# Optimization experiments

Hardware: AMD Instinct MI355X
Metric: run time of the kernel (lower is better)

## Reference

```python
import jax, jax.numpy as jnp
import numpy as np

D_MODEL = 1024
N_HEADS = 16
DFF = 4096
B, S = 2, 2048
EPS = 1e-6


def _dense_params(key, d_in, d_out):
    kw, kb = jax.random.split(key)
    w = jax.random.normal(kw, (d_in, d_out), jnp.float32) * 0.02
    b = jax.random.normal(kb, (d_out,), jnp.float32) * 0.02
    return w, b


def setup_inputs() -> dict:
    key = jax.random.key(0)
    ks = jax.random.split(key, 20)
    inp = {
        "x": jax.random.normal(ks[0], (B, S, D_MODEL), jnp.float32),
        "enc_output": jax.random.normal(ks[1], (B, S, D_MODEL), jnp.float32),
        # causal look-ahead mask: 1 where attention is NOT allowed
        "look_ahead_mask": jnp.triu(jnp.ones((S, S), jnp.float32), k=1)[None, None],
        "padding_mask": (jax.random.uniform(ks[2], (B, 1, 1, S)) < 0.1).astype(jnp.float32),
    }
    names = ["mha1_wq", "mha1_wk", "mha1_wv", "mha1_wo",
             "mha2_wq", "mha2_wk", "mha2_wv", "mha2_wo"]
    for i, n in enumerate(names):
        w, b = _dense_params(ks[3 + i], D_MODEL, D_MODEL)
        inp[n] = w
        inp[n.replace("w", "b")] = b
    inp["ffn_w1"], inp["ffn_b1"] = _dense_params(ks[11], D_MODEL, DFF)
    inp["ffn_w2"], inp["ffn_b2"] = _dense_params(ks[12], DFF, D_MODEL)
    for i, n in enumerate(["ln1", "ln2", "ln3"]):
        inp[n + "_g"] = jnp.ones((D_MODEL,), jnp.float32)
        inp[n + "_b"] = jnp.zeros((D_MODEL,), jnp.float32)
    return inp


def _layernorm(x, g, b):
    mu = jnp.mean(x, axis=-1, keepdims=True)
    var = jnp.mean(jnp.square(x - mu), axis=-1, keepdims=True)
    return (x - mu) * jax.lax.rsqrt(var + EPS) * g + b


def _mha(v, k, q, mask, wq, bq, wk, bk, wv, bv, wo, bo):
    Bq, Sq, D = q.shape
    depth = D // N_HEADS

    def split(t):  # [B,S,D] -> [B,H,S,depth]
        return t.reshape(t.shape[0], -1, N_HEADS, depth).transpose(0, 2, 1, 3)

    qh = split(q @ wq + bq)
    kh = split(k @ wk + bk)
    vh = split(v @ wv + bv)
    logits = jnp.einsum("bhqd,bhkd->bhqk", qh, kh) / jnp.sqrt(jnp.float32(depth))
    if mask is not None:
        logits = logits + mask * (-1e9)
    attn = jax.nn.softmax(logits, axis=-1)
    out = jnp.einsum("bhqk,bhkd->bhqd", attn, vh)
    out = out.transpose(0, 2, 1, 3).reshape(Bq, Sq, D)
    return out @ wo + bo


def reference(x, enc_output, look_ahead_mask, padding_mask,
              mha1_wq, mha1_bq, mha1_wk, mha1_bk, mha1_wv, mha1_bv, mha1_wo, mha1_bo,
              mha2_wq, mha2_bq, mha2_wk, mha2_bk, mha2_wv, mha2_bv, mha2_wo, mha2_bo,
              ffn_w1, ffn_b1, ffn_w2, ffn_b2,
              ln1_g, ln1_b, ln2_g, ln2_b, ln3_g, ln3_b):
    # self-attention (training=False -> dropout is identity)
    attn1 = _mha(x, x, x, look_ahead_mask,
                 mha1_wq, mha1_bq, mha1_wk, mha1_bk, mha1_wv, mha1_bv, mha1_wo, mha1_bo)
    out1 = _layernorm(x + attn1, ln1_g, ln1_b)
    # cross-attention: q from decoder, k/v from encoder output
    attn2 = _mha(enc_output, enc_output, out1, padding_mask,
                 mha2_wq, mha2_bq, mha2_wk, mha2_bk, mha2_wv, mha2_bv, mha2_wo, mha2_bo)
    out2 = _layernorm(out1 + attn2, ln2_g, ln2_b)
    ffn = jax.nn.relu(out2 @ ffn_w1 + ffn_b1) @ ffn_w2 + ffn_b2
    return _layernorm(out2 + ffn, ln3_g, ln3_b)
```

## Files before the change

kernel.cpp:

```cpp
#include <hip/hip_runtime.h>
#include <hip/hip_bf16.h>
#include <stdint.h>

#define DM   1024
#define NH   16
#define SS   2048
#define BB   2
#define MT   4096

typedef __attribute__((ext_vector_type(8))) short short8;
typedef __attribute__((ext_vector_type(4))) float f32x4;

typedef __attribute__((address_space(1))) const unsigned int as1_uint;
typedef __attribute__((address_space(3))) unsigned int as3_uint;

__device__ __forceinline__ void async16(const void* g, void* l) {
  __builtin_amdgcn_global_load_lds((as1_uint*)g, (as3_uint*)l, 16, 0, 0);
}

#define WAITV(n) asm volatile("s_waitcnt vmcnt(" #n ")" ::: "memory")
#define BARRIER_SB() do { __builtin_amdgcn_s_barrier(); __builtin_amdgcn_sched_barrier(0); } while (0)
#define EXP2(x) __builtin_amdgcn_exp2f(x)

__device__ __forceinline__ unsigned short f2bf(float f) {
  union { float f; unsigned u; } c; c.f = f;
  unsigned r = c.u + 0x7fffu + ((c.u >> 16) & 1u);
  return (unsigned short)(r >> 16);
}

__device__ __forceinline__ unsigned cvt_pk_bf16(float lo, float hi) {
  unsigned r;
  asm("v_cvt_pk_bf16_f32 %0, %1, %2" : "=v"(r) : "v"(lo), "v"(hi));
  return r;
}

__device__ __forceinline__ float swz16(float x) {
  return __uint_as_float((unsigned)__builtin_amdgcn_ds_swizzle((int)__float_as_uint(x), 0x401F));
}

__device__ __forceinline__ void xcd_swz(int& bx, int& by, int& bz) {
  int GX = gridDim.x, GY = gridDim.y;
  int nwg = GX * GY * gridDim.z;
  int old = blockIdx.x + GX * (blockIdx.y + GY * blockIdx.z);
  int f2 = (old & 7) * (nwg >> 3) + (old >> 3);
  bz = f2 / (GX * GY);
  int rem = f2 % (GX * GY);
  bx = rem / GY;
  by = rem % GY;
}

__global__ __launch_bounds__(256) void k_conv2(
    const float* __restrict__ a, const float* __restrict__ b,
    unsigned short* __restrict__ oa, unsigned short* __restrict__ ob) {
  int bxr = blockIdx.x;
  const float* in = (bxr < 4096) ? a : b;
  unsigned short* out = (bxr < 4096) ? oa : ob;
  int i = ((bxr & 4095) * 256 + threadIdx.x) * 4;
  float4 v = *(const float4*)(in + i);
  uint2 u;
  u.x = (unsigned)f2bf(v.x) | ((unsigned)f2bf(v.y) << 16);
  u.y = (unsigned)f2bf(v.z) | ((unsigned)f2bf(v.w) << 16);
  *(uint2*)(out + i) = u;
}

__global__ __launch_bounds__(256) void k_transpose_bf16(
    const float* __restrict__ in, unsigned short* __restrict__ out, int R, int C) {
  __shared__ float t[64][65];
  int c0 = blockIdx.x * 64, r0 = blockIdx.y * 64;
  int tx = threadIdx.x & 63, ty = threadIdx.x >> 6;
#pragma unroll
  for (int i = 0; i < 16; i++)
    t[ty + i * 4][tx] = in[(size_t)(r0 + ty + i * 4) * C + c0 + tx];
  __syncthreads();
#pragma unroll
  for (int i = 0; i < 16; i++)
    out[(size_t)(c0 + ty + i * 4) * R + r0 + tx] = f2bf(t[tx][ty + i * 4]);
}

struct PtrArr { const float* p[8]; };
__global__ __launch_bounds__(256) void k_transpose8(
    PtrArr ps, unsigned short* __restrict__ out0) {
  __shared__ float t[64][65];
  const float* in = ps.p[blockIdx.z];
  unsigned short* out = out0 + (size_t)blockIdx.z * 1048576;
  int c0 = blockIdx.x * 64, r0 = blockIdx.y * 64;
  int tx = threadIdx.x & 63, ty = threadIdx.x >> 6;
#pragma unroll
  for (int i = 0; i < 16; i++)
    t[ty + i * 4][tx] = in[(size_t)(r0 + ty + i * 4) * 1024 + c0 + tx];
  __syncthreads();
#pragma unroll
  for (int i = 0; i < 16; i++)
    out[(size_t)(c0 + ty + i * 4) * 1024 + r0 + tx] = f2bf(t[tx][ty + i * 4]);
}

__device__ __forceinline__ void stage_half(
    unsigned short* lds, int dst_off, const unsigned short* __restrict__ src,
    int sbase, int c0, int K, int kk, int tid) {
#pragma unroll
  for (int c = 0; c < 2; c++) {
    int e = ((c0 + c) * 512 + tid) * 8;
    int r_ = e >> 6, s_ = e & 63;
    async16(src + (size_t)(sbase + r_) * K + kk + (s_ ^ ((r_ & 4) << 2)),
            &lds[dst_off + e]);
  }
}

__device__ __forceinline__ void read_afrags(
    const unsigned short* lds, int aoff, int wm, int rh, int l15, int l4,
    short8 af[4][2]) {
#pragma unroll
  for (int i = 0; i < 4; i++) {
    int arow = wm * 128 + rh * 64 + i * 16 + l15;
#pragma unroll
    for (int ks = 0; ks < 2; ks++)
      af[i][ks] = *(const short8*)&lds[aoff + arow * 64 +
          ((ks * 32 + l4 * 8) ^ ((arow & 4) << 2))];
  }
}

__device__ __forceinline__ void read_bfrags(
    const unsigned short* lds, int boff, int wn, int ch, int l15, int l4,
    short8 bf[2][2]) {
#pragma unroll
  for (int j = 0; j < 2; j++) {
    int brw = wn * 64 + ch * 32 + j * 16 + l15;
#pragma unroll
    for (int ks = 0; ks < 2; ks++)
      bf[j][ks] = *(const short8*)&lds[boff + brw * 64 +
          ((ks * 32 + l4 * 8) ^ ((brw & 4) << 2))];
  }
}

#define MFMA_CL(RH, CH)                                                        \
  __builtin_amdgcn_s_barrier();                                                \
  asm volatile("s_waitcnt lgkmcnt(0)" ::: "memory");                           \
  __builtin_amdgcn_sched_barrier(0);                                           \
  __builtin_amdgcn_s_setprio(1);                                               \
  _Pragma("unroll")                                                            \
  for (int ks = 0; ks < 2; ks++)                                               \
    _Pragma("unroll")                                                          \
    for (int i = 0; i < 4; i++)                                                \
      _Pragma("unroll")                                                        \
      for (int j = 0; j < 2; j++)                                              \
        acc[(RH) * 4 + i][(CH) * 2 + j] =                                      \
            __builtin_amdgcn_mfma_f32_16x16x32_bf16(                           \
                af[i][ks], bf[j][ks], acc[(RH) * 4 + i][(CH) * 2 + j], 0, 0, 0); \
  __builtin_amdgcn_s_setprio(0);

template<int OUT_MODE, bool RELU>
__global__ __launch_bounds__(512, 2) void k_gemm256(
    const unsigned short* __restrict__ A,
    const unsigned short* __restrict__ Bt,
    const float* __restrict__ bias,
    void* __restrict__ p0, void* __restrict__ p1,
    void* __restrict__ p2, void* __restrict__ p3,
    int M, int N, int K, int KS) {
  extern __shared__ unsigned short lds[];
  int tid = threadIdx.x;
  int wid = tid >> 6, lane = tid & 63;
  int wm = wid >> 2, wn = wid & 3;
  int l15 = lane & 15, l4 = lane >> 4;
  int brow = blockIdx.y * 256, bcol = blockIdx.x * 256;
  int bz = blockIdx.z;
  int kbeg = bz * KS;
  int nk = KS / 64;

  f32x4 acc[8][4];
#pragma unroll
  for (int i = 0; i < 8; i++)
#pragma unroll
    for (int j = 0; j < 4; j++) acc[i][j] = (f32x4){0.f, 0.f, 0.f, 0.f};

  short8 af[4][2], bf[2][2];

  stage_half(lds, 32768, Bt, bcol, 0, K, kbeg, tid);
  stage_half(lds, 32768, Bt, bcol, 2, K, kbeg, tid);
  stage_half(lds, 0,     A,  brow, 0, K, kbeg, tid);
  stage_half(lds, 0,     A,  brow, 2, K, kbeg, tid);
  WAITV(0);
  __builtin_amdgcn_s_barrier();

  for (int t = 0; t < nk; t++) {
    int buf = t & 1, nb = buf ^ 1;
    int aoff = buf * 16384, boff = 32768 + buf * 16384;
    int naoff = nb * 16384, nboff = 32768 + nb * 16384;
    int kk2 = kbeg + (t + 1) * 64;
    bool more = (t + 1 < nk);

    read_afrags(lds, aoff, wm, 0, l15, l4, af);
    read_bfrags(lds, boff, wn, 0, l15, l4, bf);
    if (more) {
      stage_half(lds, nboff, Bt, bcol, 0, K, kk2, tid);
      stage_half(lds, nboff, Bt, bcol, 2, K, kk2, tid);
    }
    MFMA_CL(0, 0);
    __builtin_amdgcn_s_barrier();

    read_bfrags(lds, boff, wn, 1, l15, l4, bf);
    if (more) stage_half(lds, naoff, A, brow, 0, K, kk2, tid);
    MFMA_CL(0, 1);
    __builtin_amdgcn_s_barrier();

    read_afrags(lds, aoff, wm, 1, l15, l4, af);
    read_bfrags(lds, boff, wn, 0, l15, l4, bf);
    if (more) stage_half(lds, naoff, A, brow, 2, K, kk2, tid);
    MFMA_CL(1, 0);
    __builtin_amdgcn_s_barrier();

    read_bfrags(lds, boff, wn, 1, l15, l4, bf);
    MFMA_CL(1, 1);
    if (more) {
      WAITV(0);
      __builtin_amdgcn_s_barrier();
    }
  }

  if (OUT_MODE == 1) {
    unsigned short* op = (unsigned short*)p0;
#pragma unroll
    for (int ai = 0; ai < 8; ai++)
#pragma unroll
      for (int bj = 0; bj < 4; bj++) {
        int row = brow + wm * 128 + ai * 16 + l4 * 4;
        int col = bcol + wn * 64 + bj * 16 + l15;
        float bs = bias[col];
#pragma unroll
        for (int r = 0; r < 4; r++) {
          float v = acc[ai][bj][r] + bs;
          if (RELU) v = fmaxf(v, 0.f);
          op[(size_t)(row + r) * N + col] = f2bf(v);
        }
      }
  } else {
    float* op = (float*)((bz == 0) ? p0 : (bz == 1) ? p1 : (bz == 2) ? p2 : p3);
#pragma unroll
    for (int ai = 0; ai < 8; ai++)
#pragma unroll
      for (int bj = 0; bj < 4; bj++) {
        int row = brow + wm * 128 + ai * 16 + l4 * 4;
        int col = bcol + wn * 64 + bj * 16 + l15;
#pragma unroll
        for (int r = 0; r < 4; r++)
          op[(size_t)(row + r) * N + col] = acc[ai][bj][r];
      }
  }
}

template<int BM, int OUT_MODE, bool RELU, bool RESID, bool SPLITK>
__global__ __launch_bounds__(256) void k_gemm(
    const unsigned short* __restrict__ A,
    const unsigned short* __restrict__ Bt,
    const float* __restrict__ bias,
    const float* __restrict__ resid,
    void* __restrict__ outp, void* __restrict__ outp2,
    int M, int N, int K, int KS) {
  __shared__ unsigned short Alds[3][BM * 32];
  __shared__ unsigned short Blds[3][128 * 32];
  int tid = threadIdx.x;
  int w = tid >> 6, lane = tid & 63;
  int l15 = lane & 15, l4 = lane >> 4;
  int bxs, bys, bzs;
  xcd_swz(bxs, bys, bzs);
  int brow = bys * BM, bcol = bxs * 128;

  constexpr int MR = 4;
  constexpr int NR = (BM == 128) ? 4 : 2;
  int wr = (BM == 128) ? (w >> 1) : 0;
  int wc = (BM == 128) ? (w & 1) : w;
  int rbase = wr * 64;
  int cbase = wc * (NR * 16);

  f32x4 acc[MR][NR];
#pragma unroll
  for (int i = 0; i < MR; i++)
#pragma unroll
    for (int j = 0; j < NR; j++) acc[i][j] = (f32x4){0.f, 0.f, 0.f, 0.f};

#define STAGEG(bufi, kk) do {                                                  \
    _Pragma("unroll")                                                          \
    for (int c = 0; c < BM / 64; c++) {                                        \
      int elem = (c * 256 + tid) * 8;                                          \
      int row = elem >> 5, col = elem & 31;                                    \
      async16(A + (size_t)(brow + row) * K + (kk) + col, &Alds[bufi][elem]);   \
    }                                                                          \
    _Pragma("unroll")                                                          \
    for (int c = 0; c < 2; c++) {                                              \
      int elem = (c * 256 + tid) * 8;                                          \
      int row = elem >> 5, col = elem & 31;                                    \
      async16(Bt + (size_t)(bcol + row) * K + (kk) + col, &Blds[bufi][elem]);  \
    } } while (0)

  int kbeg = SPLITK ? bzs * KS : 0;
  int nk = KS / 32;
  STAGEG(0, kbeg);
  if (nk > 1) {
    STAGEG(1, kbeg + 32);
    if (BM == 128) WAITV(4); else WAITV(3);
  } else {
    WAITV(0);
  }
  BARRIER_SB();

  for (int t = 0; t < nk; t++) {
    int buf = t % 3;
    if (t + 2 < nk) STAGEG((t + 2) % 3, kbeg + (t + 2) * 32);
    short8 af[MR], bfr[NR];
#pragma unroll
    for (int i = 0; i < MR; i++)
      af[i] = *(const short8*)&Alds[buf][(rbase + i * 16 + l15) * 32 + l4 * 8];
#pragma unroll
    for (int j = 0; j < NR; j++)
      bfr[j] = *(const short8*)&Blds[buf][(cbase + j * 16 + l15) * 32 + l4 * 8];
#pragma unroll
    for (int i = 0; i < MR; i++)
#pragma unroll
      for (int j = 0; j < NR; j++)
        acc[i][j] = __builtin_amdgcn_mfma_f32_16x16x32_bf16(af[i], bfr[j], acc[i][j], 0, 0, 0);
    if (t + 2 < nk) {
      if (BM == 128) WAITV(4); else WAITV(3);
    } else if (t + 1 < nk) {
      WAITV(0);
    }
    if (t + 1 < nk) BARRIER_SB();
  }
#undef STAGEG

  void* op = (SPLITK && bzs) ? outp2 : outp;
#pragma unroll
  for (int i = 0; i < MR; i++)
#pragma unroll
    for (int j = 0; j < NR; j++) {
      int row = brow + rbase + i * 16 + l4 * 4;
      int col = bcol + cbase + j * 16 + l15;
      float bs = (SPLITK || !bias) ? 0.f : bias[col];
#pragma unroll
      for (int r = 0; r < 4; r++) {
        float v = acc[i][j][r] + bs;
        if (RESID) v += resid[(size_t)(row + r) * N + col];
        if (RELU) v = fmaxf(v, 0.f);
        if (OUT_MODE == 0) ((float*)op)[(size_t)(row + r) * N + col] = v;
        else               ((unsigned short*)op)[(size_t)(row + r) * N + col] = f2bf(v);
      }
    }
}

__global__ __launch_bounds__(256) void k_gemm_qkv(
    const unsigned short* __restrict__ a0, const unsigned short* __restrict__ a1,
    const unsigned short* __restrict__ a2,
    const unsigned short* __restrict__ Bt,
    const float* __restrict__ b0, const float* __restrict__ b1, const float* __restrict__ b2,
    unsigned short* __restrict__ o0, unsigned short* __restrict__ o1, unsigned short* __restrict__ o2,
    int vmat, int M, int K) {
  __shared__ unsigned short Alds[3][128 * 32];
  __shared__ unsigned short Blds[3][128 * 32];
  int tid = threadIdx.x;
  int w = tid >> 6, lane = tid & 63;
  int wr = w >> 1, wc = w & 1;
  int l15 = lane & 15, l4 = lane >> 4;
  int bxs, bys, z;
  xcd_swz(bxs, bys, z);
  const unsigned short* A  = (z == 0) ? a0 : (z == 1) ? a1 : a2;
  const unsigned short* Bz = Bt + (size_t)z * 1048576;
  int brow = bys * 128, bcol = bxs * 128;

  f32x4 acc[4][4];
#pragma unroll
  for (int i = 0; i < 4; i++)
#pragma unroll
    for (int j = 0; j < 4; j++) acc[i][j] = (f32x4){0.f, 0.f, 0.f, 0.f};

#define STAGEQ(bufi, kk) do {                                                  \
    _Pragma("unroll")                                                          \
    for (int c = 0; c < 2; c++) {                                              \
      int elem = (c * 256 + tid) * 8;                                          \
      int row = elem >> 5, col = elem & 31;                                    \
      async16(A + (size_t)(brow + row) * K + (kk) + col, &Alds[bufi][elem]);   \
      async16(Bz + (size_t)(bcol + row) * K + (kk) + col, &Blds[bufi][elem]);  \
    } } while (0)

  int nk = K / 32;
  STAGEQ(0, 0);
  STAGEQ(1, 32);
  WAITV(4);
  BARRIER_SB();

  for (int t = 0; t < nk; t++) {
    int buf = t % 3;
    if (t + 2 < nk) STAGEQ((t + 2) % 3, (t + 2) * 32);
    short8 af[4], bfr[4];
#pragma unroll
    for (int i = 0; i < 4; i++) {
      af[i]  = *(const short8*)&Alds[buf][(wr * 64 + i * 16 + l15) * 32 + l4 * 8];
      bfr[i] = *(const short8*)&Blds[buf][(wc * 64 + i * 16 + l15) * 32 + l4 * 8];
    }
#pragma unroll
    for (int i = 0; i < 4; i++)
#pragma unroll
      for (int j = 0; j < 4; j++)
        acc[i][j] = __builtin_amdgcn_mfma_f32_16x16x32_bf16(af[i], bfr[j], acc[i][j], 0, 0, 0);
    if (t + 2 < nk) WAITV(4);
    else if (t + 1 < nk) WAITV(0);
    if (t + 1 < nk) BARRIER_SB();
  }
#undef STAGEQ

  const float* bias = (z == 0) ? b0 : (z == 1) ? b1 : b2;
  unsigned short* op = (z == 0) ? o0 : (z == 1) ? o1 : o2;
  bool tr = (z == vmat);
#pragma unroll
  for (int i = 0; i < 4; i++)
#pragma unroll
    for (int j = 0; j < 4; j++) {
      int row = brow + wr * 64 + i * 16 + l4 * 4;
      int colL = bcol + wc * 64 + j * 16 + l15;
      float bs = bias[colL];
#pragma unroll
      for (int r = 0; r < 4; r++) {
        float v = acc[i][j][r] + bs;
        if (tr) op[(size_t)colL * M + row + r] = f2bf(v);
        else    op[(size_t)(row + r) * 1024 + colL] = f2bf(v);
      }
    }
}

template<bool CAUSAL, int NF>
__global__ __launch_bounds__(256) void k_attn(
    const unsigned short* __restrict__ Q,
    const unsigned short* __restrict__ Kb,
    const unsigned short* __restrict__ Vt,
    const float* __restrict__ pm,
    unsigned short* __restrict__ out) {
  __shared__ unsigned short Klds[3][64 * 64];
  __shared__ unsigned short Vlds[3][64 * 64];
  __shared__ unsigned short Pw[4][NF][16 * 72];
  int tid = threadIdx.x, w = tid >> 6, lane = tid & 63;
  int l15 = lane & 15, l4 = lane >> 4;
  int h = blockIdx.y, b = blockIdx.z;
  const float SC = 0.125f * 1.44269504089f;
  const int NPASS = CAUSAL ? 2 : 1;

#define STAGE(bufi, kt_) do {                                                  \
    _Pragma("unroll")                                                          \
    for (int c = 0; c < 2; c++) {                                              \
      int e0 = w * 1024 + c * 512;                                             \
      int elem = e0 + lane * 8;                                                \
      int row_ = elem >> 6;                                                    \
      int col_ = (elem & 63) ^ ((row_ & 7) << 3);                              \
      async16(Kb + (size_t)(b * SS + (kt_) * 64 + row_) * DM + h * 64 + col_,  \
              &Klds[bufi][elem]);                                              \
      async16(Vt + (size_t)(h * 64 + row_) * MT + b * SS + (kt_) * 64 + col_,  \
              &Vlds[bufi][elem]);                                              \
    } } while (0)

  for (int pass = 0; pass < NPASS; pass++) {
    int qt = CAUSAL ? (pass == 0 ? (31 - (int)blockIdx.x) : (int)blockIdx.x)
                    : (int)blockIdx.x;
    int qbase = qt * (NF * 64) + w * (NF * 16);

    short8 qf[NF][2];
#pragma unroll
    for (int f = 0; f < NF; f++) {
      size_t qrow = (size_t)b * SS + qbase + f * 16 + l15;
#pragma unroll
      for (int ks = 0; ks < 2; ks++)
        qf[f][ks] = *(const short8*)(Q + qrow * DM + h * 64 + ks * 32 + l4 * 8);
    }

    float mrow[NF], lrow[NF];
    f32x4 accO[NF][4];
#pragma unroll
    for (int f = 0; f < NF; f++) {
      mrow[f] = -1e30f; lrow[f] = 0.f;
#pragma unroll
      for (int d = 0; d < 4; d++) accO[f][d] = (f32x4){0.f, 0.f, 0.f, 0.f};
    }

    int ktend = CAUSAL ? qt : (SS / 64 - 1);
    if (pass) BARRIER_SB();
    STAGE(0, 0);
    if (ktend >= 1) { STAGE(1, 1); WAITV(4); } else { WAITV(0); }
    BARRIER_SB();

    for (int kt = 0; kt <= ktend; kt++) {
      int buf = kt % 3;
      if (kt + 2 <= ktend) STAGE((kt + 2) % 3, kt + 2);

      bool active = !CAUSAL || (kt * 64 <= qbase + NF * 16 - 1);
      if (active) {
        f32x4 sa[NF][4];
#pragma unroll
        for (int f = 0; f < NF; f++)
#pragma unroll
          for (int nt = 0; nt < 4; nt++) sa[f][nt] = (f32x4){0.f, 0.f, 0.f, 0.f};
        __builtin_amdgcn_s_setprio(1);
#pragma unroll
        for (int ks = 0; ks < 2; ks++)
#pragma unroll
          for (int nt = 0; nt < 4; nt++) {
            int kr = nt * 16 + l15;
            short8 kf = *(const short8*)&Klds[buf][kr * 64 + ((ks * 32 + l4 * 8) ^ ((kr & 7) << 3))];
#pragma unroll
            for (int f = 0; f < NF; f++)
              sa[f][nt] = __builtin_amdgcn_mfma_f32_16x16x32_bf16(kf, qf[f][ks], sa[f][nt], 0, 0, 0);
          }
        __builtin_amdgcn_s_setprio(0);

        float pmb[16];
        if (!CAUSAL) {
#pragma unroll
          for (int nt = 0; nt < 4; nt++) {
            float4 pmv = *(const float4*)(pm + b * SS + kt * 64 + nt * 16 + l4 * 4);
#pragma unroll
            for (int r = 0; r < 4; r++) pmb[nt * 4 + r] = ((const float*)&pmv)[r] * -1e30f;
          }
        }
        bool diag = CAUSAL && (kt * 64 + 63 > qbase);

        float sv[NF][16], tm[NF];
#pragma unroll
        for (int f = 0; f < NF; f++) {
          if (CAUSAL && !diag) {
#pragma unroll
            for (int i = 0; i < 16; i++) sv[f][i] = sa[f][i >> 2][i & 3] * SC;
          } else if (CAUSAL) {
#pragma unroll
            for (int nt = 0; nt < 4; nt++)
#pragma unroll
              for (int r = 0; r < 4; r++) {
                float s = sa[f][nt][r] * SC;
                int kg = kt * 64 + nt * 16 + l4 * 4 + r;
                int qg = qbase + f * 16 + l15;
                if (kg > qg) s = -1e30f;
                sv[f][nt * 4 + r] = s;
              }
          } else {
#pragma unroll
            for (int i = 0; i < 16; i++)
              sv[f][i] = fmaf(sa[f][i >> 2][i & 3], SC, pmb[i]);
          }
          float t8[8];
#pragma unroll
          for (int i = 0; i < 8; i++) t8[i] = fmaxf(sv[f][i], sv[f][i + 8]);
#pragma unroll
          for (int i = 0; i < 4; i++) t8[i] = fmaxf(t8[i], t8[i + 4]);
          t8[0] = fmaxf(t8[0], t8[1]);
          t8[2] = fmaxf(t8[2], t8[3]);
          tm[f] = fmaxf(t8[0], t8[2]);
        }

        float sA[NF];
#pragma unroll
        for (int f = 0; f < NF; f++) sA[f] = swz16(tm[f]);
#pragma unroll
        for (int f = 0; f < NF; f++) tm[f] = fmaxf(tm[f], sA[f]);
        float xA[NF];
#pragma unroll
        for (int f = 0; f < NF; f++) xA[f] = __shfl_xor(tm[f], 32);
#pragma unroll
        for (int f = 0; f < NF; f++) tm[f] = fmaxf(tm[f], xA[f]);

#pragma unroll
        for (int f = 0; f < NF; f++) {
          if (!__all(tm[f] - mrow[f] <= 8.f)) {
            float mnew = fmaxf(mrow[f], tm[f]);
            float corr = EXP2(mrow[f] - mnew);
            mrow[f] = mnew;
            lrow[f] *= corr;
#pragma unroll
            for (int r = 0; r < 4; r++) {
              float cq = __shfl(corr, l4 * 4 + r);
#pragma unroll
              for (int dt = 0; dt < 4; dt++) accO[f][dt][r] *= cq;
            }
          }

          float p[16];
#pragma unroll
          for (int i = 0; i < 16; i++) p[i] = EXP2(sv[f][i] - mrow[f]);
          float a8[8];
#pragma unroll
          for (int i = 0; i < 8; i++) a8[i] = p[i] + p[i + 8];
#pragma unroll
          for (int i = 0; i < 4; i++) a8[i] = a8[i] + a8[i + 4];
          lrow[f] += (a8[0] + a8[1]) + (a8[2] + a8[3]);

#pragma unroll
          for (int nt = 0; nt < 4; nt++) {
            uint2 u;
            u.x = cvt_pk_bf16(p[nt * 4 + 0], p[nt * 4 + 1]);
            u.y = cvt_pk_bf16(p[nt * 4 + 2], p[nt * 4 + 3]);
            *(uint2*)&Pw[w][f][l15 * 72 + nt * 16 + l4 * 4] = u;
          }
        }

        __builtin_amdgcn_s_setprio(1);
#pragma unroll
        for (int ks = 0; ks < 2; ks++) {
          short8 pf[NF];
#pragma unroll
          for (int f = 0; f < NF; f++)
            pf[f] = *(const short8*)&Pw[w][f][l15 * 72 + ks * 32 + l4 * 8];
#pragma unroll
          for (int dt = 0; dt < 4; dt++) {
            int vr = dt * 16 + l15;
            short8 vf = *(const short8*)&Vlds[buf][vr * 64 + ((ks * 32 + l4 * 8) ^ ((vr & 7) << 3))];
#pragma unroll
            for (int f = 0; f < NF; f++)
              accO[f][dt] = __builtin_amdgcn_mfma_f32_16x16x32_bf16(pf[f], vf, accO[f][dt], 0, 0, 0);
          }
        }
        __builtin_amdgcn_s_setprio(0);
      }

      if (kt + 2 <= ktend) WAITV(4);
      else if (kt + 1 <= ktend) WAITV(0);
      if (kt + 1 <= ktend) BARRIER_SB();
    }

#pragma unroll
    for (int f = 0; f < NF; f++) {
      lrow[f] += swz16(lrow[f]);
      lrow[f] += __shfl_xor(lrow[f], 32);
    }
#pragma unroll
    for (int f = 0; f < NF; f++)
#pragma unroll
      for (int r = 0; r < 4; r++) {
        float lq = __shfl(lrow[f], l4 * 4 + r);
        float inv = 1.f / lq;
        size_t row = (size_t)b * SS + qbase + f * 16 + l4 * 4 + r;
#pragma unroll
        for (int dt = 0; dt < 4; dt++)
          out[row * DM + h * 64 + dt * 16 + l15] = f2bf(accO[f][dt][r] * inv);
      }
  }
#undef STAGE
}

__global__ __launch_bounds__(256) void k_ln(
    const float* __restrict__ in, const float* __restrict__ in2,
    const float* __restrict__ in3, const float* __restrict__ in4,
    const float* __restrict__ resid, const float* __restrict__ bias,
    const float* __restrict__ g, const float* __restrict__ bb,
    float* __restrict__ outf, unsigned short* __restrict__ outb) {
  int row = blockIdx.x, tid = threadIdx.x;
  int w = tid >> 6;
  __shared__ float red[4];
  float4 v = *(const float4*)(in + (size_t)row * 1024 + tid * 4);
  if (in2) {
    float4 v2 = *(const float4*)(in2 + (size_t)row * 1024 + tid * 4);
    v.x += v2.x; v.y += v2.y; v.z += v2.z; v.w += v2.w;
  }
  if (in3) {
    float4 v2 = *(const float4*)(in3 + (size_t)row * 1024 + tid * 4);
    v.x += v2.x; v.y += v2.y; v.z += v2.z; v.w += v2.w;
  }
  if (in4) {
    float4 v2 = *(const float4*)(in4 + (size_t)row * 1024 + tid * 4);
    v.x += v2.x; v.y += v2.y; v.z += v2.z; v.w += v2.w;
  }
  if (resid) {
    float4 v2 = *(const float4*)(resid + (size_t)row * 1024 + tid * 4);
    v.x += v2.x; v.y += v2.y; v.z += v2.z; v.w += v2.w;
  }
  if (bias) {
    float4 v2 = *(const float4*)(bias + tid * 4);
    v.x += v2.x; v.y += v2.y; v.z += v2.z; v.w += v2.w;
  }
  float s = v.x + v.y + v.z + v.w;
#pragma unroll
  for (int d = 1; d < 64; d <<= 1) s += __shfl_xor(s, d);
  if ((tid & 63) == 0) red[w] = s;
  __syncthreads();
  float mu = (red[0] + red[1] + red[2] + red[3]) * (1.f / 1024.f);
  float d0 = v.x - mu, d1 = v.y - mu, d2 = v.z - mu, d3 = v.w - mu;
  float q = d0 * d0 + d1 * d1 + d2 * d2 + d3 * d3;
#pragma unroll
  for (int d = 1; d < 64; d <<= 1) q += __shfl_xor(q, d);
  __syncthreads();
  if ((tid & 63) == 0) red[w] = q;
  __syncthreads();
  float var = (red[0] + red[1] + red[2] + red[3]) * (1.f / 1024.f);
  float rs = rsqrtf(var + 1e-6f);
  float4 gg = *(const float4*)(g + tid * 4);
  float4 bv = *(const float4*)(bb + tid * 4);
  float y0 = d0 * rs * gg.x + bv.x;
  float y1 = d1 * rs * gg.y + bv.y;
  float y2 = d2 * rs * gg.z + bv.z;
  float y3 = d3 * rs * gg.w + bv.w;
  if (outf) {
    float4 o; o.x = y0; o.y = y1; o.z = y2; o.w = y3;
    *(float4*)(outf + (size_t)row * 1024 + tid * 4) = o;
  }
  if (outb) {
    uint2 u;
    u.x = (unsigned)f2bf(y0) | ((unsigned)f2bf(y1) << 16);
    u.y = (unsigned)f2bf(y2) | ((unsigned)f2bf(y3) << 16);
    *(uint2*)(outb + (size_t)row * 1024 + tid * 4) = u;
  }
}

extern "C" void kernel_launch(void* const* d_in, const int* in_sizes, int n_in,
                              void* d_out, int out_size, void* d_ws, size_t ws_size,
                              hipStream_t stream) {
  const float* x    = (const float*)d_in[0];
  const float* enc  = (const float*)d_in[1];
  const float* pm   = (const float*)d_in[3];
  const float* wq1  = (const float*)d_in[4];   const float* bq1 = (const float*)d_in[5];
  const float* wk1  = (const float*)d_in[6];   const float* bk1 = (const float*)d_in[7];
  const float* wv1  = (const float*)d_in[8];   const float* bv1 = (const float*)d_in[9];
  const float* wo1  = (const float*)d_in[10];  const float* bo1 = (const float*)d_in[11];
  const float* wq2  = (const float*)d_in[12];  const float* bq2 = (const float*)d_in[13];
  const float* wk2  = (const float*)d_in[14];  const float* bk2 = (const float*)d_in[15];
  const float* wv2  = (const float*)d_in[16];  const float* bv2 = (const float*)d_in[17];
  const float* wo2  = (const float*)d_in[18];  const float* bo2 = (const float*)d_in[19];
  const float* fw1  = (const float*)d_in[20];  const float* fb1 = (const float*)d_in[21];
  const float* fw2  = (const float*)d_in[22];  const float* fb2 = (const float*)d_in[23];
  const float* ln1g = (const float*)d_in[24];  const float* ln1b = (const float*)d_in[25];
  const float* ln2g = (const float*)d_in[26];  const float* ln2b = (const float*)d_in[27];
  const float* ln3g = (const float*)d_in[28];  const float* ln3b = (const float*)d_in[29];

  char* ws = (char*)d_ws;
  unsigned short* XB = (unsigned short*)(ws + 0);
  unsigned short* EB = (unsigned short*)(ws + 8388608);
  unsigned short* Qb = (unsigned short*)(ws + 16777216);
  unsigned short* Kb = (unsigned short*)(ws + 25165824);
  unsigned short* Vt = (unsigned short*)(ws + 33554432);
  unsigned short* AT = (unsigned short*)(ws + 41943040);
  float*          T  = (float*)(ws + 50331648);
  float*          R  = (float*)(ws + 67108864);
  unsigned short* RB = (unsigned short*)(ws + 83886080);
  unsigned short* WT0 = (unsigned short*)(ws + 92274688);
  unsigned short* W1T = (unsigned short*)(ws + 92274688 + 16777216);
  unsigned short* W2T = (unsigned short*)(ws + 92274688 + 25165824);
  unsigned short* H   = (unsigned short*)(ws + 0);
  float*          T1  = (float*)(ws + 33554432);
  float*          T1o = (float*)(ws + 16777216);
  float*          P0  = T;
  float*          P1  = (float*)(ws + 33554432);
  float*          P2  = (float*)(ws + 83886080);
  float*          P3  = (float*)(ws + 100663296);

  k_conv2<<<8192, 256, 0, stream>>>(x, enc, XB, EB);
  PtrArr ptrs;
  ptrs.p[0] = wq1; ptrs.p[1] = wk1; ptrs.p[2] = wv1; ptrs.p[3] = wo1;
  ptrs.p[4] = wq2; ptrs.p[5] = wk2; ptrs.p[6] = wv2; ptrs.p[7] = wo2;
  k_transpose8<<<dim3(16, 16, 8), 256, 0, stream>>>(ptrs, WT0);
  k_transpose_bf16<<<dim3(64, 16), 256, 0, stream>>>(fw1, W1T, 1024, 4096);
  k_transpose_bf16<<<dim3(16, 64), 256, 0, stream>>>(fw2, W2T, 4096, 1024);

  k_gemm_qkv<<<dim3(8, 32, 3), 256, 0, stream>>>(XB, XB, XB, WT0, bq1, bk1, bv1,
                                                 Qb, Kb, Vt, 2, MT, DM);
  k_attn<true, 1><<<dim3(16, 16, 2), 256, 0, stream>>>(Qb, Kb, Vt, nullptr, AT);
  k_gemm<64, 0, false, false, true><<<dim3(8, 64, 2), 256, 0, stream>>>(
      AT, WT0 + 3 * 1048576, nullptr, nullptr, T, T1o, MT, DM, DM, 512);
  k_ln<<<4096, 256, 0, stream>>>(T, T1o, nullptr, nullptr, x, bo1, ln1g, ln1b, R, RB);

  k_gemm_qkv<<<dim3(8, 32, 3), 256, 0, stream>>>(RB, EB, EB, WT0 + 4 * 1048576,
                                                 bq2, bk2, bv2, Qb, Kb, Vt, 2, MT, DM);
  k_attn<false, 2><<<dim3(16, 16, 2), 256, 0, stream>>>(Qb, Kb, Vt, pm, AT);
  k_gemm<64, 0, false, false, true><<<dim3(8, 64, 2), 256, 0, stream>>>(
      AT, WT0 + 7 * 1048576, nullptr, nullptr, T, T1o, MT, DM, DM, 512);
  k_ln<<<4096, 256, 0, stream>>>(T, T1o, nullptr, nullptr, R, bo2, ln2g, ln2b, R, RB);

  hipError_t ea = hipFuncSetAttribute(
      reinterpret_cast<const void*>(k_gemm256<1, true>),
      hipFuncAttributeMaxDynamicSharedMemorySize, 131072);
  hipError_t eb = hipFuncSetAttribute(
      reinterpret_cast<const void*>(k_gemm256<0, false>),
      hipFuncAttributeMaxDynamicSharedMemorySize, 131072);
  if (ea == hipSuccess && eb == hipSuccess) {
    k_gemm256<1, true><<<dim3(16, 16, 1), 512, 131072, stream>>>(
        RB, W1T, fb1, H, nullptr, nullptr, nullptr, MT, 4096, DM, DM);
    k_gemm256<0, false><<<dim3(4, 16, 4), 512, 131072, stream>>>(
        H, W2T, nullptr, P0, P1, P2, P3, MT, DM, 4096, 1024);
    k_ln<<<4096, 256, 0, stream>>>(P0, P1, P2, P3, R, fb2, ln3g, ln3b,
                                   (float*)d_out, nullptr);
  } else {
    k_gemm<128, 1, true, false, false><<<dim3(32, 32), 256, 0, stream>>>(
        RB, W1T, fb1, nullptr, H, nullptr, MT, 4096, DM, 1024);
    k_gemm<64, 0, false, false, true><<<dim3(8, 64, 2), 256, 0, stream>>>(
        H, W2T, nullptr, nullptr, T, T1, MT, DM, 4096, 2048);
    k_ln<<<4096, 256, 0, stream>>>(T, T1, nullptr, nullptr, R, fb2, ln3g, ln3b,
                                   (float*)d_out, nullptr);
  }
}
```

Measured before the change: 431.1 us.

## Use 256x256 GEMM tiles for QKV and output projections, fold softmax scale into Q

Adds a 256x256-tile, 512-thread QKV projection kernel that shares the existing k_gemm256 main loop, now factored into a macro. The attention output projections also move to k_gemm256 with split-K of 2. The softmax scale, including log2e, is folded into the Q projection epilogue, which removes a per-logit multiply inside attention. The goal is better data reuse and fewer attention ALU ops. The trade-off is a small grid of 192 or 128 blocks, which may underfill the GPU.

```diff
diff --git a/kernel.cpp b/kernel.cpp
--- a/kernel.cpp
+++ b/kernel.cpp
@@ -21,6 +21,7 @@
 #define WAITV(n) asm volatile("s_waitcnt vmcnt(" #n ")" ::: "memory")
 #define BARRIER_SB() do { __builtin_amdgcn_s_barrier(); __builtin_amdgcn_sched_barrier(0); } while (0)
 #define EXP2(x) __builtin_amdgcn_exp2f(x)
+#define QSCALE 0.180336879f
 
 __device__ __forceinline__ unsigned short f2bf(float f) {
   union { float f; unsigned u; } c; c.f = f;
@@ -36,6 +37,17 @@
 
 __device__ __forceinline__ float swz16(float x) {
   return __uint_as_float((unsigned)__builtin_amdgcn_ds_swizzle((int)__float_as_uint(x), 0x401F));
+}
+
+__device__ __forceinline__ float max16(const float* s) {
+  float a = fmaxf(fmaxf(s[0], s[1]), s[2]);
+  float b = fmaxf(fmaxf(s[3], s[4]), s[5]);
+  float c = fmaxf(fmaxf(s[6], s[7]), s[8]);
+  float d = fmaxf(fmaxf(s[9], s[10]), s[11]);
+  float e = fmaxf(fmaxf(s[12], s[13]), s[14]);
+  float ab = fmaxf(fmaxf(a, b), c);
+  float de = fmaxf(fmaxf(d, e), s[15]);
+  return fmaxf(ab, de);
 }
 
 __device__ __forceinline__ void xcd_swz(int& bx, int& by, int& bz) {
@@ -147,6 +159,44 @@
             __builtin_amdgcn_mfma_f32_16x16x32_bf16(                           \
                 af[i][ks], bf[j][ks], acc[(RH) * 4 + i][(CH) * 2 + j], 0, 0, 0); \
   __builtin_amdgcn_s_setprio(0);
+
+#define GEMM256_LOOP(Asrc, Bsrc, ROWB, COLB)                                   \
+  stage_half(lds, 32768, Bsrc, COLB, 0, K, kbeg, tid);                         \
+  stage_half(lds, 32768, Bsrc, COLB, 2, K, kbeg, tid);                         \
+  stage_half(lds, 0,     Asrc, ROWB, 0, K, kbeg, tid);                         \
+  stage_half(lds, 0,     Asrc, ROWB, 2, K, kbeg, tid);                         \
+  WAITV(0);                                                                    \
+  __builtin_amdgcn_s_barrier();                                                \
+  for (int t = 0; t < nk; t++) {                                               \
+    int buf = t & 1, nb = buf ^ 1;                                             \
+    int aoff = buf * 16384, boff = 32768 + buf * 16384;                        \
+    int naoff = nb * 16384, nboff = 32768 + nb * 16384;                        \
+    int kk2 = kbeg + (t + 1) * 64;                                             \
+    bool more = (t + 1 < nk);                                                  \
+    read_afrags(lds, aoff, wm, 0, l15, l4, af);                                \
+    read_bfrags(lds, boff, wn, 0, l15, l4, bf);                                \
+    if (more) {                                                                \
+      stage_half(lds, nboff, Bsrc, COLB, 0, K, kk2, tid);                      \
+      stage_half(lds, nboff, Bsrc, COLB, 2, K, kk2, tid);                      \
+    }                                                                          \
+    MFMA_CL(0, 0);                                                             \
+    __builtin_amdgcn_s_barrier();                                              \
+    read_bfrags(lds, boff, wn, 1, l15, l4, bf);                                \
+    if (more) stage_half(lds, naoff, Asrc, ROWB, 0, K, kk2, tid);              \
+    MFMA_CL(0, 1);                                                             \
+    __builtin_amdgcn_s_barrier();                                              \
+    read_afrags(lds, aoff, wm, 1, l15, l4, af);                                \
+    read_bfrags(lds, boff, wn, 0, l15, l4, bf);                                \
+    if (more) stage_half(lds, naoff, Asrc, ROWB, 2, K, kk2, tid);              \
+    MFMA_CL(1, 0);                                                             \
+    __builtin_amdgcn_s_barrier();                                              \
+    read_bfrags(lds, boff, wn, 1, l15, l4, bf);                                \
+    MFMA_CL(1, 1);                                                             \
+    if (more) {                                                                \
+      WAITV(0);                                                                \
+      __builtin_amdgcn_s_barrier();                                            \
+    }                                                                          \
+  }
 
 template<int OUT_MODE, bool RELU>
 __global__ __launch_bounds__(512, 2) void k_gemm256(
@@ -171,50 +221,9 @@
   for (int i = 0; i < 8; i++)
 #pragma unroll
     for (int j = 0; j < 4; j++) acc[i][j] = (f32x4){0.f, 0.f, 0.f, 0.f};
-
   short8 af[4][2], bf[2][2];
 
-  stage_half(lds, 32768, Bt, bcol, 0, K, kbeg, tid);
-  stage_half(lds, 32768, Bt, bcol, 2, K, kbeg, tid);
-  stage_half(lds, 0,     A,  brow, 0, K, kbeg, tid);
-  stage_half(lds, 0,     A,  brow, 2, K, kbeg, tid);
-  WAITV(0);
-  __builtin_amdgcn_s_barrier();
-
-  for (int t = 0; t < nk; t++) {
-    int buf = t & 1, nb = buf ^ 1;
-    int aoff = buf * 16384, boff = 32768 + buf * 16384;
-    int naoff = nb * 16384, nboff = 32768 + nb * 16384;
-    int kk2 = kbeg + (t + 1) * 64;
-    bool more = (t + 1 < nk);
-
-    read_afrags(lds, aoff, wm, 0, l15, l4, af);
-    read_bfrags(lds, boff, wn, 0, l15, l4, bf);
-    if (more) {
-      stage_half(lds, nboff, Bt, bcol, 0, K, kk2, tid);
-      stage_half(lds, nboff, Bt, bcol, 2, K, kk2, tid);
-    }
-    MFMA_CL(0, 0);
-    __builtin_amdgcn_s_barrier();
-
-    read_bfrags(lds, boff, wn, 1, l15, l4, bf);
-    if (more) stage_half(lds, naoff, A, brow, 0, K, kk2, tid);
-    MFMA_CL(0, 1);
-    __builtin_amdgcn_s_barrier();
-
-    read_afrags(lds, aoff, wm, 1, l15, l4, af);
-    read_bfrags(lds, boff, wn, 0, l15, l4, bf);
-    if (more) stage_half(lds, naoff, A, brow, 2, K, kk2, tid);
-    MFMA_CL(1, 0);
-    __builtin_amdgcn_s_barrier();
-
-    read_bfrags(lds, boff, wn, 1, l15, l4, bf);
-    MFMA_CL(1, 1);
-    if (more) {
-      WAITV(0);
-      __builtin_amdgcn_s_barrier();
-    }
-  }
+  GEMM256_LOOP(A, Bt, brow, bcol);
 
   if (OUT_MODE == 1) {
     unsigned short* op = (unsigned short*)p0;
@@ -245,6 +254,55 @@
           op[(size_t)(row + r) * N + col] = acc[ai][bj][r];
       }
   }
+}
+
+__global__ __launch_bounds__(512, 2) void k_qkv256(
+    const unsigned short* __restrict__ a0, const unsigned short* __restrict__ a1,
+    const unsigned short* __restrict__ a2,
+    const unsigned short* __restrict__ Bt,
+    const float* __restrict__ b0, const float* __restrict__ b1, const float* __restrict__ b2,
+    unsigned short* __restrict__ o0, unsigned short* __restrict__ o1,
+    unsigned short* __restrict__ o2,
+    int vmat, float qscale, int M, int K) {
+  extern __shared__ unsigned short lds[];
+  int tid = threadIdx.x;
+  int wid = tid >> 6, lane = tid & 63;
+  int wm = wid >> 2, wn = wid & 3;
+  int l15 = lane & 15, l4 = lane >> 4;
+  int z = blockIdx.z;
+  const unsigned short* A  = (z == 0) ? a0 : (z == 1) ? a1 : a2;
+  const unsigned short* Bz = Bt + (size_t)z * 1048576;
+  int brow = blockIdx.y * 256, bcol = blockIdx.x * 256;
+  int kbeg = 0;
+  int nk = K / 64;
+
+  f32x4 acc[8][4];
+#pragma unroll
+  for (int i = 0; i < 8; i++)
+#pragma unroll
+    for (int j = 0; j < 4; j++) acc[i][j] = (f32x4){0.f, 0.f, 0.f, 0.f};
+  short8 af[4][2], bf[2][2];
+
+  GEMM256_LOOP(A, Bz, brow, bcol);
+
+  const float* bias = (z == 0) ? b0 : (z == 1) ? b1 : b2;
+  unsigned short* op = (z == 0) ? o0 : (z == 1) ? o1 : o2;
+  bool tr = (z == vmat);
+#pragma unroll
+  for (int ai = 0; ai < 8; ai++)
+#pragma unroll
+    for (int bj = 0; bj < 4; bj++) {
+      int row = brow + wm * 128 + ai * 16 + l4 * 4;
+      int col = bcol + wn * 64 + bj * 16 + l15;
+      float bs = bias[col];
+#pragma unroll
+      for (int r = 0; r < 4; r++) {
+        float v = acc[ai][bj][r] + bs;
+        if (z == 0) v *= qscale;
+        if (tr) op[(size_t)col * M + row + r] = f2bf(v);
+        else    op[(size_t)(row + r) * 1024 + col] = f2bf(v);
+      }
+    }
 }
 
 template<int BM, int OUT_MODE, bool RELU, bool RESID, bool SPLITK>
@@ -351,7 +409,7 @@
     const unsigned short* __restrict__ Bt,
     const float* __restrict__ b0, const float* __restrict__ b1, const float* __restrict__ b2,
     unsigned short* __restrict__ o0, unsigned short* __restrict__ o1, unsigned short* __restrict__ o2,
-    int vmat, int M, int K) {
+    int vmat, float qscale, int M, int K) {
   __shared__ unsigned short Alds[3][128 * 32];
   __shared__ unsigned short Blds[3][128 * 32];
   int tid = threadIdx.x;
@@ -418,6 +476,7 @@
 #pragma unroll
       for (int r = 0; r < 4; r++) {
         float v = acc[i][j][r] + bs;
+        if (z == 0) v *= qscale;
         if (tr) op[(size_t)colL * M + row + r] = f2bf(v);
         else    op[(size_t)(row + r) * 1024 + colL] = f2bf(v);
       }
@@ -437,7 +496,6 @@
   int tid = threadIdx.x, w = tid >> 6, lane = tid & 63;
   int l15 = lane & 15, l4 = lane >> 4;
   int h = blockIdx.y, b = blockIdx.z;
-  const float SC = 0.125f * 1.44269504089f;
   const int NPASS = CAUSAL ? 2 : 1;
 
 #define STAGE(bufi, kt_) do {                                                  \
@@ -522,13 +580,13 @@
         for (int f = 0; f < NF; f++) {
           if (CAUSAL && !diag) {
 #pragma unroll
-            for (int i = 0; i < 16; i++) sv[f][i] = sa[f][i >> 2][i & 3] * SC;
+            for (int i = 0; i < 16; i++) sv[f][i] = sa[f][i >> 2][i & 3];
           } else if (CAUSAL) {
 #pragma unroll
             for (int nt = 0; nt < 4; nt++)
 #pragma unroll
               for (int r = 0; r < 4; r++) {
-                float s = sa[f][nt][r] * SC;
+                float s = sa[f][nt][r];
                 int kg = kt * 64 + nt * 16 + l4 * 4 + r;
                 int qg = qbase + f * 16 + l15;
                 if (kg > qg) s = -1e30f;
@@ -537,16 +595,9 @@
           } else {
 #pragma unroll
             for (int i = 0; i < 16; i++)
-              sv[f][i] = fmaf(sa[f][i >> 2][i & 3], SC, pmb[i]);
+              sv[f][i] = sa[f][i >> 2][i & 3] + pmb[i];
           }
-          float t8[8];
-#pragma unroll
-          for (int i = 0; i < 8; i++) t8[i] = fmaxf(sv[f][i], sv[f][i + 8]);
-#pragma unroll
-          for (int i = 0; i < 4; i++) t8[i] = fmaxf(t8[i], t8[i + 4]);
-          t8[0] = fmaxf(t8[0], t8[1]);
-          t8[2] = fmaxf(t8[2], t8[3]);
-          tm[f] = fmaxf(t8[0], t8[2]);
+          tm[f] = max16(sv[f]);
         }
 
         float sA[NF];
@@ -735,7 +786,6 @@
   unsigned short* W1T = (unsigned short*)(ws + 92274688 + 16777216);
   unsigned short* W2T = (unsigned short*)(ws + 92274688 + 25165824);
   unsigned short* H   = (unsigned short*)(ws + 0);
-  float*          T1  = (float*)(ws + 33554432);
   float*          T1o = (float*)(ws + 16777216);
   float*          P0  = T;
   float*          P1  = (float*)(ws + 33554432);
@@ -750,27 +800,48 @@
   k_transpose_bf16<<<dim3(64, 16), 256, 0, stream>>>(fw1, W1T, 1024, 4096);
   k_transpose_bf16<<<dim3(16, 64), 256, 0, stream>>>(fw2, W2T, 4096, 1024);
 
-  k_gemm_qkv<<<dim3(8, 32, 3), 256, 0, stream>>>(XB, XB, XB, WT0, bq1, bk1, bv1,
-                                                 Qb, Kb, Vt, 2, MT, DM);
-  k_attn<true, 1><<<dim3(16, 16, 2), 256, 0, stream>>>(Qb, Kb, Vt, nullptr, AT);
-  k_gemm<64, 0, false, false, true><<<dim3(8, 64, 2), 256, 0, stream>>>(
-      AT, WT0 + 3 * 1048576, nullptr, nullptr, T, T1o, MT, DM, DM, 512);
-  k_ln<<<4096, 256, 0, stream>>>(T, T1o, nullptr, nullptr, x, bo1, ln1g, ln1b, R, RB);
-
-  k_gemm_qkv<<<dim3(8, 32, 3), 256, 0, stream>>>(RB, EB, EB, WT0 + 4 * 1048576,
-                                                 bq2, bk2, bv2, Qb, Kb, Vt, 2, MT, DM);
-  k_attn<false, 2><<<dim3(16, 16, 2), 256, 0, stream>>>(Qb, Kb, Vt, pm, AT);
-  k_gemm<64, 0, false, false, true><<<dim3(8, 64, 2), 256, 0, stream>>>(
-      AT, WT0 + 7 * 1048576, nullptr, nullptr, T, T1o, MT, DM, DM, 512);
-  k_ln<<<4096, 256, 0, stream>>>(T, T1o, nullptr, nullptr, R, bo2, ln2g, ln2b, R, RB);
-
-  hipError_t ea = hipFuncSetAttribute(
+  hipError_t e1 = hipFuncSetAttribute(
       reinterpret_cast<const void*>(k_gemm256<1, true>),
       hipFuncAttributeMaxDynamicSharedMemorySize, 131072);
-  hipError_t eb = hipFuncSetAttribute(
+  hipError_t e2 = hipFuncSetAttribute(
       reinterpret_cast<const void*>(k_gemm256<0, false>),
       hipFuncAttributeMaxDynamicSharedMemorySize, 131072);
-  if (ea == hipSuccess && eb == hipSuccess) {
+  hipError_t e3 = hipFuncSetAttribute(
+      reinterpret_cast<const void*>(k_qkv256),
+      hipFuncAttributeMaxDynamicSharedMemorySize, 131072);
+  bool big = (e1 == hipSuccess && e2 == hipSuccess && e3 == hipSuccess);
+
+  if (big)
+    k_qkv256<<<dim3(4, 16, 3), 512, 131072, stream>>>(
+        XB, XB, XB, WT0, bq1, bk1, bv1, Qb, Kb, Vt, 2, QSCALE, MT, DM);
+  else
+    k_gemm_qkv<<<dim3(8, 32, 3), 256, 0, stream>>>(XB, XB, XB, WT0, bq1, bk1, bv1,
+                                                   Qb, Kb, Vt, 2, QSCALE, MT, DM);
+  k_attn<true, 1><<<dim3(16, 16, 2), 256, 0, stream>>>(Qb, Kb, Vt, nullptr, AT);
+  if (big)
+    k_gemm256<0, false><<<dim3(4, 16, 2), 512, 131072, stream>>>(
+        AT, WT0 + 3 * 1048576, nullptr, T, T1o, nullptr, nullptr, MT, DM, DM, 512);
+  else
+    k_gemm<64, 0, false, false, true><<<dim3(8, 64, 2), 256, 0, stream>>>(
+        AT, WT0 + 3 * 1048576, nullptr, nullptr, T, T1o, MT, DM, DM, 512);
+  k_ln<<<4096, 256, 0, stream>>>(T, T1o, nullptr, nullptr, x, bo1, ln1g, ln1b, R, RB);
+
+  if (big)
+    k_qkv256<<<dim3(4, 16, 3), 512, 131072, stream>>>(
+        RB, EB, EB, WT0 + 4 * 1048576, bq2, bk2, bv2, Qb, Kb, Vt, 2, QSCALE, MT, DM);
+  else
+    k_gemm_qkv<<<dim3(8, 32, 3), 256, 0, stream>>>(RB, EB, EB, WT0 + 4 * 1048576,
+                                                   bq2, bk2, bv2, Qb, Kb, Vt, 2, QSCALE, MT, DM);
+  k_attn<false, 2><<<dim3(16, 16, 2), 256, 0, stream>>>(Qb, Kb, Vt, pm, AT);
+  if (big)
+    k_gemm256<0, false><<<dim3(4, 16, 2), 512, 131072, stream>>>(
+        AT, WT0 + 7 * 1048576, nullptr, T, T1o, nullptr, nullptr, MT, DM, DM, 512);
+  else
+    k_gemm<64, 0, false, false, true><<<dim3(8, 64, 2), 256, 0, stream>>>(
+        AT, WT0 + 7 * 1048576, nullptr, nullptr, T, T1o, MT, DM, DM, 512);
+  k_ln<<<4096, 256, 0, stream>>>(T, T1o, nullptr, nullptr, R, bo2, ln2g, ln2b, R, RB);
+
+  if (big) {
     k_gemm256<1, true><<<dim3(16, 16, 1), 512, 131072, stream>>>(
         RB, W1T, fb1, H, nullptr, nullptr, nullptr, MT, 4096, DM, DM);
     k_gemm256<0, false><<<dim3(4, 16, 4), 512, 131072, stream>>>(
@@ -781,8 +852,8 @@
     k_gemm<128, 1, true, false, false><<<dim3(32, 32), 256, 0, stream>>>(
         RB, W1T, fb1, nullptr, H, nullptr, MT, 4096, DM, 1024);
     k_gemm<64, 0, false, false, true><<<dim3(8, 64, 2), 256, 0, stream>>>(
-        H, W2T, nullptr, nullptr, T, T1, MT, DM, 4096, 2048);
-    k_ln<<<4096, 256, 0, stream>>>(T, T1, nullptr, nullptr, R, fb2, ln3g, ln3b,
-                                   (float*)d_out, nullptr);
-  }
-}
+        H, W2T, nullptr, nullptr, T, (float*)(ws + 33554432), MT, DM, 4096, 2048);
+    k_ln<<<4096, 256, 0, stream>>>(T, (float*)(ws + 33554432), nullptr, nullptr,
+                                   R, fb2, ln3g, ln3b, (float*)d_out, nullptr);
+  }
+}
```

After: 457.7 us. 1.06x slower.
